# Optimization experiments

Hardware: AMD Instinct MI355X
Metric: run time of the kernel (lower is better)

Reference implementation:

```python
import jax, jax.numpy as jnp
import numpy as np

IGNORE_INDEX = -100
LSE_SQUARE_SCALE = 1e-4  # z_loss coefficient


def setup_inputs() -> dict:
    key = jax.random.key(0)
    k1, k2, k3, k4 = jax.random.split(key, 4)
    N, D, V = 4096, 2048, 50257
    inp = {
        "input": jax.random.normal(k1, (N, D), dtype=jnp.float32),
        "weight": jax.random.normal(k2, (V, D), dtype=jnp.float32) * (D ** -0.5),
        "bias": jnp.zeros((V,), dtype=jnp.float32),
        "target": jax.random.randint(k3, (N,), 0, V, dtype=jnp.int64),
    }
    return inp


def reference(input, weight, bias, target):
    # logits: [N, V] = input @ weight.T + bias  (the GEMM the fused kernel chunks)
    logits = jnp.einsum("nd,vd->nv", input, weight) + bias
    lse = jax.nn.logsumexp(logits, axis=-1)  # [N]
    valid = target != IGNORE_INDEX
    safe_tgt = jnp.where(valid, target, 0)
    tgt_logit = jnp.take_along_axis(logits, safe_tgt[:, None], axis=-1)[:, 0]
    ce = lse - tgt_logit                      # per-token cross entropy
    z = LSE_SQUARE_SCALE * lse * lse          # per-token z-loss (lse_square_scale * lse^2)
    per_token = jnp.where(valid, ce + z, 0.0)
    n_valid = jnp.maximum(jnp.sum(valid), 1).astype(per_token.dtype)
    loss = jnp.sum(per_token) / n_valid       # mean over non-ignored tokens (includes z-loss)
    z_loss = jnp.sum(jnp.where(valid, z, 0.0)) / n_valid
    return loss, z_loss
```

## Files before the change

kernel.cpp:

```cpp
#include <hip/hip_runtime.h>
#include <stdint.h>

#define N_TOK 4096
#define DIM   2048
#define VOCAB 50257
#define VPAD  50432
#define IGNORE_IDX (-100)

typedef short  bf16x8 __attribute__((ext_vector_type(8)));
typedef float  f32x4  __attribute__((ext_vector_type(4)));
typedef unsigned short u16x8 __attribute__((ext_vector_type(8)));

typedef const __attribute__((address_space(1))) unsigned int* gptr_t;
typedef __attribute__((address_space(3))) unsigned int*       lptr_t;

__device__ __forceinline__ unsigned short f2bf(float f) {
  union { float f; uint32_t u; } c; c.f = f;
  uint32_t u = c.u;
  return (unsigned short)((u + 0x7FFFu + ((u >> 16) & 1u)) >> 16);
}

__global__ void cvt_weight(const float* __restrict__ w, unsigned short* __restrict__ o) {
  const int t   = blockIdx.x * 256 + threadIdx.x;
  const int idx = t << 3;
  const int v   = idx >> 11;
  u16x8 r = {0, 0, 0, 0, 0, 0, 0, 0};
  if (v < VOCAB) {
    const float4* p = (const float4*)(w + idx);
    const float4 x0 = p[0];
    const float4 x1 = p[1];
    r[0] = f2bf(x0.x); r[1] = f2bf(x0.y); r[2] = f2bf(x0.z); r[3] = f2bf(x0.w);
    r[4] = f2bf(x1.x); r[5] = f2bf(x1.y); r[6] = f2bf(x1.z); r[7] = f2bf(x1.w);
  }
  *(u16x8*)(o + idx) = r;
}

__global__ void cvt_input(const float* __restrict__ a, unsigned short* __restrict__ o) {
  const int t   = blockIdx.x * 256 + threadIdx.x;
  const int idx = t << 3;
  const float4* p = (const float4*)(a + idx);
  const float4 x0 = p[0];
  const float4 x1 = p[1];
  u16x8 r;
  r[0] = f2bf(x0.x); r[1] = f2bf(x0.y); r[2] = f2bf(x0.z); r[3] = f2bf(x0.w);
  r[4] = f2bf(x1.x); r[5] = f2bf(x1.y); r[6] = f2bf(x1.z); r[7] = f2bf(x1.w);
  *(u16x8*)(o + idx) = r;
}


#define STAGE_A(nb, ko) do { \
  __builtin_amdgcn_global_load_lds((gptr_t)(const void*)(ag + 0 * 64 * DIM + (ko)), (lptr_t)(void*)(&As[nb][(0 * 512 + tid) * 8]), 16, 0, 0); \
  __builtin_amdgcn_global_load_lds((gptr_t)(const void*)(ag + 1 * 64 * DIM + (ko)), (lptr_t)(void*)(&As[nb][(1 * 512 + tid) * 8]), 16, 0, 0); \
  __builtin_amdgcn_global_load_lds((gptr_t)(const void*)(ag + 2 * 64 * DIM + (ko)), (lptr_t)(void*)(&As[nb][(2 * 512 + tid) * 8]), 16, 0, 0); \
  __builtin_amdgcn_global_load_lds((gptr_t)(const void*)(ag + 3 * 64 * DIM + (ko)), (lptr_t)(void*)(&As[nb][(3 * 512 + tid) * 8]), 16, 0, 0); \
} while (0)

#define STAGE_B0(nb, ko) do { \
  __builtin_amdgcn_global_load_lds((gptr_t)(const void*)(bg + 0 * 64 * DIM + (ko)), (lptr_t)(void*)(&Bs[nb][(0 * 512 + tid) * 8]), 16, 0, 0); \
  __builtin_amdgcn_global_load_lds((gptr_t)(const void*)(bg + 1 * 64 * DIM + (ko)), (lptr_t)(void*)(&Bs[nb][(1 * 512 + tid) * 8]), 16, 0, 0); \
} while (0)

#define STAGE_B1(nb, ko) do { \
  __builtin_amdgcn_global_load_lds((gptr_t)(const void*)(bg + 2 * 64 * DIM + (ko)), (lptr_t)(void*)(&Bs[nb][(2 * 512 + tid) * 8]), 16, 0, 0); \
  __builtin_amdgcn_global_load_lds((gptr_t)(const void*)(bg + 3 * 64 * DIM + (ko)), (lptr_t)(void*)(&Bs[nb][(3 * 512 + tid) * 8]), 16, 0, 0); \
} while (0)

#define LOAD_AV(mq) do { \
  _Pragma("unroll") \
  for (int fm = 0; fm < 4; ++fm) { \
    av[fm][0] = *(const bf16x8*)(Ab + ((mq) * 64 + fm * 16) * 64 + kx0); \
    av[fm][1] = *(const bf16x8*)(Ab + ((mq) * 64 + fm * 16) * 64 + kx1); \
  } \
} while (0)

#define LOAD_BV(nq) do { \
  _Pragma("unroll") \
  for (int fn = 0; fn < 2; ++fn) { \
    bv[nq][fn][0] = *(const bf16x8*)(Bb + ((nq) * 32 + fn * 16) * 64 + kx0); \
    bv[nq][fn][1] = *(const bf16x8*)(Bb + ((nq) * 32 + fn * 16) * 64 + kx1); \
  } \
} while (0)

#define MFMA16(mq, nq) do { \
  _Pragma("unroll") \
  for (int fm = 0; fm < 4; ++fm) \
    _Pragma("unroll") \
    for (int fn = 0; fn < 2; ++fn) { \
      acc[(mq) * 4 + fm][(nq) * 2 + fn] = __builtin_amdgcn_mfma_f32_16x16x32_bf16(av[fm][0], bv[nq][fn][0], acc[(mq) * 4 + fm][(nq) * 2 + fn], 0, 0, 0); \
      acc[(mq) * 4 + fm][(nq) * 2 + fn] = __builtin_amdgcn_mfma_f32_16x16x32_bf16(av[fm][1], bv[nq][fn][1], acc[(mq) * 4 + fm][(nq) * 2 + fn], 0, 0, 0); \
    } \
} while (0)

#define PHASE(mq, nq, DOA, DOB, STAGE_STMT) do { \
  if (DOA) LOAD_AV(mq); \
  if (DOB) LOAD_BV(nq); \
  STAGE_STMT; \
  __builtin_amdgcn_s_barrier(); \
  asm volatile("s_waitcnt lgkmcnt(0)" ::: "memory"); \
  __builtin_amdgcn_s_setprio(1); \
  MFMA16(mq, nq); \
  __builtin_amdgcn_s_setprio(0); \
  __builtin_amdgcn_s_barrier(); \
} while (0)

__global__ __launch_bounds__(512, 2) void flce_gemm(
    const unsigned short* __restrict__ A,
    const unsigned short* __restrict__ B,
    const float* __restrict__ bias,
    const int* __restrict__ target,
    float* __restrict__ sumexp,
    float* __restrict__ tgtlog)
{
  __shared__ unsigned short As[2][256 * 64];
  __shared__ unsigned short Bs[2][256 * 64];

  const int tid  = threadIdx.x;
  const int lane = tid & 63;
  const int wave = tid >> 6;
  const int wm   = wave >> 2;
  const int wn   = wave & 3;

  const int bid = blockIdx.x;
  const int swz = (bid & 7) * (3152 / 8) + (bid >> 3);
  const int m0  = (swz & 15) * 256;
  const int v0  = (swz >> 4) * 256;

  const int mrow = lane & 15;
  const int quad = lane >> 4;

  const int srow = tid >> 3;
  const int scg  = (tid ^ (tid >> 3)) & 7;
  const unsigned short* ag = A + (size_t)(m0 + srow) * DIM + scg * 8;
  const unsigned short* bg = B + (size_t)(v0 + srow) * DIM + scg * 8;

  const int kx0 = (((0 * 64) + quad * 16) ^ ((mrow & 7) << 4)) >> 1;
  const int kx1 = (((1 * 64) + quad * 16) ^ ((mrow & 7) << 4)) >> 1;

  f32x4 acc[8][4];
#pragma unroll
  for (int i = 0; i < 8; i++)
#pragma unroll
    for (int j = 0; j < 4; j++) acc[i][j] = (f32x4){0.f, 0.f, 0.f, 0.f};

  bf16x8 av[4][2];
  bf16x8 bv[2][2][2];

  STAGE_A(0, 0);
  STAGE_B0(0, 0);
  STAGE_B1(0, 0);

  int cb = 0;
#pragma unroll 1
  for (int t = 0; t < 31; ++t) {
    const int nb = cb ^ 1;
    const int ko = (t + 1) * 64;
    STAGE_A(nb, ko);
    asm volatile("s_waitcnt vmcnt(4)" ::: "memory");
    __builtin_amdgcn_s_barrier();
    asm volatile("" ::: "memory");
    const unsigned short* Ab = &As[cb][(wm * 128 + mrow) * 64];
    const unsigned short* Bb = &Bs[cb][(wn * 64 + mrow) * 64];
    PHASE(0, 0, 1, 1, STAGE_B0(nb, ko));
    PHASE(0, 1, 0, 1, STAGE_B1(nb, ko));
    PHASE(1, 0, 1, 0, (void)0);
    PHASE(1, 1, 0, 0, (void)0);
    cb = nb;
  }
  asm volatile("s_waitcnt vmcnt(0)" ::: "memory");
  __builtin_amdgcn_s_barrier();
  asm volatile("" ::: "memory");
  {
    const unsigned short* Ab = &As[cb][(wm * 128 + mrow) * 64];
    const unsigned short* Bb = &Bs[cb][(wn * 64 + mrow) * 64];
    PHASE(0, 0, 1, 1, (void)0);
    PHASE(0, 1, 0, 1, (void)0);
    PHASE(1, 0, 1, 0, (void)0);
    PHASE(1, 1, 0, 0, (void)0);
  }

  const int colb = v0 + wn * 64;
#pragma unroll
  for (int i = 0; i < 8; ++i) {
    const int rowl = wm * 128 + i * 16 + quad * 4;
    const int4 tg = *(const int4*)(target + m0 + rowl);
    float rs[4] = {0.f, 0.f, 0.f, 0.f};
#pragma unroll
    for (int j = 0; j < 4; ++j) {
      const int colg = colb + j * 16 + mrow;
      if (colg < VOCAB) {
        const float bvv = bias[colg];
#pragma unroll
        for (int r = 0; r < 4; ++r) {
          const float lg = acc[i][j][r] + bvv;
          rs[r] += __expf(lg);
          const int tgr = (r == 0) ? tg.x : (r == 1) ? tg.y : (r == 2) ? tg.z : tg.w;
          if (tgr == colg) tgtlog[m0 + rowl + r] = lg;
        }
      }
    }
#pragma unroll
    for (int r = 0; r < 4; ++r) {
      float v = rs[r];
      v += __shfl_xor(v, 1);
      v += __shfl_xor(v, 2);
      v += __shfl_xor(v, 4);
      v += __shfl_xor(v, 8);
      if (mrow == 0) atomicAdd(&sumexp[m0 + rowl + r], v);
    }
  }
}

__global__ void flce_final(const float* __restrict__ sumexp,
                           const float* __restrict__ tgtlog,
                           const int* __restrict__ target,
                           float* __restrict__ out) {
  const int tid = threadIdx.x;
  float ls = 0.f, zs = 0.f;
  int cnt = 0;
  for (int r = tid; r < N_TOK; r += 256) {
    const int t = target[r];
    if (t != IGNORE_IDX) {
      const float lse = logf(sumexp[r]);
      const float z = 1e-4f * lse * lse;
      ls += (lse - tgtlog[r]) + z;
      zs += z;
      cnt++;
    }
  }
#pragma unroll
  for (int off = 32; off > 0; off >>= 1) {
    ls += __shfl_down(ls, off);
    zs += __shfl_down(zs, off);
    cnt += __shfl_down(cnt, off);
  }
  __shared__ float sls[4], szs[4];
  __shared__ int scnt[4];
  const int lane = tid & 63, wv = tid >> 6;
  if (lane == 0) { sls[wv] = ls; szs[wv] = zs; scnt[wv] = cnt; }
  __syncthreads();
  if (tid == 0) {
    float L = 0.f, Z = 0.f;
    int C = 0;
    for (int w = 0; w < 4; w++) { L += sls[w]; Z += szs[w]; C += scnt[w]; }
    const float n = (float)(C > 0 ? C : 1);
    out[0] = L / n;
    out[1] = Z / n;
  }
}

extern "C" void kernel_launch(void* const* d_in, const int* in_sizes, int n_in,
                              void* d_out, int out_size, void* d_ws, size_t ws_size,
                              hipStream_t stream) {
  const float* input  = (const float*)d_in[0];
  const float* weight = (const float*)d_in[1];
  const float* bias   = (const float*)d_in[2];
  const int*   target = (const int*)d_in[3];
  float* out = (float*)d_out;

  unsigned short* wbf = (unsigned short*)d_ws;
  unsigned short* abf = wbf + (size_t)VPAD * DIM;
  float* sumexp = (float*)(abf + (size_t)N_TOK * DIM);
  float* tgtlog = sumexp + N_TOK;

  hipMemsetAsync(sumexp, 0, N_TOK * sizeof(float), stream);
  cvt_weight<<<(VPAD * DIM) / 2048, 256, 0, stream>>>(weight, wbf);
  cvt_input<<<(N_TOK * DIM) / 2048, 256, 0, stream>>>(input, abf);
  flce_gemm<<<(N_TOK / 256) * (VPAD / 256), 512, 0, stream>>>(abf, wbf, bias, target, sumexp, tgtlog);
  flce_final<<<1, 256, 0, stream>>>(sumexp, tgtlog, target, out);
}
```

Before: 1.705 ms.

## Issue all tile loads up front and trim per-phase barriers in GEMM loop

```diff
diff --git a/kernel.cpp b/kernel.cpp
--- a/kernel.cpp
+++ b/kernel.cpp
@@ -48,19 +48,13 @@
 }
 
 
-#define STAGE_A(nb, ko) do { \
+#define STAGE_ALL(nb, ko) do { \
   __builtin_amdgcn_global_load_lds((gptr_t)(const void*)(ag + 0 * 64 * DIM + (ko)), (lptr_t)(void*)(&As[nb][(0 * 512 + tid) * 8]), 16, 0, 0); \
   __builtin_amdgcn_global_load_lds((gptr_t)(const void*)(ag + 1 * 64 * DIM + (ko)), (lptr_t)(void*)(&As[nb][(1 * 512 + tid) * 8]), 16, 0, 0); \
   __builtin_amdgcn_global_load_lds((gptr_t)(const void*)(ag + 2 * 64 * DIM + (ko)), (lptr_t)(void*)(&As[nb][(2 * 512 + tid) * 8]), 16, 0, 0); \
   __builtin_amdgcn_global_load_lds((gptr_t)(const void*)(ag + 3 * 64 * DIM + (ko)), (lptr_t)(void*)(&As[nb][(3 * 512 + tid) * 8]), 16, 0, 0); \
-} while (0)
-
-#define STAGE_B0(nb, ko) do { \
   __builtin_amdgcn_global_load_lds((gptr_t)(const void*)(bg + 0 * 64 * DIM + (ko)), (lptr_t)(void*)(&Bs[nb][(0 * 512 + tid) * 8]), 16, 0, 0); \
   __builtin_amdgcn_global_load_lds((gptr_t)(const void*)(bg + 1 * 64 * DIM + (ko)), (lptr_t)(void*)(&Bs[nb][(1 * 512 + tid) * 8]), 16, 0, 0); \
-} while (0)
-
-#define STAGE_B1(nb, ko) do { \
   __builtin_amdgcn_global_load_lds((gptr_t)(const void*)(bg + 2 * 64 * DIM + (ko)), (lptr_t)(void*)(&Bs[nb][(2 * 512 + tid) * 8]), 16, 0, 0); \
   __builtin_amdgcn_global_load_lds((gptr_t)(const void*)(bg + 3 * 64 * DIM + (ko)), (lptr_t)(void*)(&Bs[nb][(3 * 512 + tid) * 8]), 16, 0, 0); \
 } while (0)
@@ -91,16 +85,11 @@
     } \
 } while (0)
 
-#define PHASE(mq, nq, DOA, DOB, STAGE_STMT) do { \
-  if (DOA) LOAD_AV(mq); \
-  if (DOB) LOAD_BV(nq); \
-  STAGE_STMT; \
+#define MFMA_PHASE(mq, nq) do { \
   __builtin_amdgcn_s_barrier(); \
-  asm volatile("s_waitcnt lgkmcnt(0)" ::: "memory"); \
   __builtin_amdgcn_s_setprio(1); \
   MFMA16(mq, nq); \
   __builtin_amdgcn_s_setprio(0); \
-  __builtin_amdgcn_s_barrier(); \
 } while (0)
 
 __global__ __launch_bounds__(512, 2) void flce_gemm(
@@ -145,37 +134,34 @@
   bf16x8 av[4][2];
   bf16x8 bv[2][2][2];
 
-  STAGE_A(0, 0);
-  STAGE_B0(0, 0);
-  STAGE_B1(0, 0);
+  STAGE_ALL(0, 0);
 
   int cb = 0;
 #pragma unroll 1
-  for (int t = 0; t < 31; ++t) {
+  for (int t = 0; t < 32; ++t) {
     const int nb = cb ^ 1;
-    const int ko = (t + 1) * 64;
-    STAGE_A(nb, ko);
-    asm volatile("s_waitcnt vmcnt(4)" ::: "memory");
+    if (t < 31) {
+      STAGE_ALL(nb, (t + 1) * 64);
+      asm volatile("s_waitcnt vmcnt(8)" ::: "memory");
+    } else {
+      asm volatile("s_waitcnt vmcnt(0)" ::: "memory");
+    }
     __builtin_amdgcn_s_barrier();
     asm volatile("" ::: "memory");
+
     const unsigned short* Ab = &As[cb][(wm * 128 + mrow) * 64];
     const unsigned short* Bb = &Bs[cb][(wn * 64 + mrow) * 64];
-    PHASE(0, 0, 1, 1, STAGE_B0(nb, ko));
-    PHASE(0, 1, 0, 1, STAGE_B1(nb, ko));
-    PHASE(1, 0, 1, 0, (void)0);
-    PHASE(1, 1, 0, 0, (void)0);
+
+    LOAD_AV(0);
+    LOAD_BV(0);
+    MFMA_PHASE(0, 0);
+    LOAD_BV(1);
+    MFMA_PHASE(0, 1);
+    LOAD_AV(1);
+    MFMA_PHASE(1, 0);
+    MFMA_PHASE(1, 1);
+
     cb = nb;
-  }
-  asm volatile("s_waitcnt vmcnt(0)" ::: "memory");
-  __builtin_amdgcn_s_barrier();
-  asm volatile("" ::: "memory");
-  {
-    const unsigned short* Ab = &As[cb][(wm * 128 + mrow) * 64];
-    const unsigned short* Bb = &Bs[cb][(wn * 64 + mrow) * 64];
-    PHASE(0, 0, 1, 1, (void)0);
-    PHASE(0, 1, 0, 1, (void)0);
-    PHASE(1, 0, 1, 0, (void)0);
-    PHASE(1, 1, 0, 0, (void)0);
   }
 
   const int colb = v0 + wn * 64;
```

After: 1.690 ms. Within noise of the previous version (-0.9%).
